# Kernel optimization log

Measured on AMD Instinct MI355X. Metric: run time of the kernel, lower is better.

Reference implementation:

```python
import jax, jax.numpy as jnp
import numpy as np

B, T, C_IN, H, NC = 256, 512, 64, 256, 6


def setup_inputs() -> dict:
    key = jax.random.key(0)
    ks = jax.random.split(key, 12)
    s = 0.05  # init scale for stability
    return {
        "x":    jax.random.normal(ks[0], (B, T, C_IN), dtype=jnp.float32),
        "Wih0": jax.random.normal(ks[1], (4 * H, C_IN), dtype=jnp.float32) * s,
        "Whh0": jax.random.normal(ks[2], (4 * H, H), dtype=jnp.float32) * s,
        "bih0": jax.random.normal(ks[3], (4 * H,), dtype=jnp.float32) * s,
        "bhh0": jax.random.normal(ks[4], (4 * H,), dtype=jnp.float32) * s,
        "Wih1": jax.random.normal(ks[5], (4 * H, H), dtype=jnp.float32) * s,
        "Whh1": jax.random.normal(ks[6], (4 * H, H), dtype=jnp.float32) * s,
        "bih1": jax.random.normal(ks[7], (4 * H,), dtype=jnp.float32) * s,
        "bhh1": jax.random.normal(ks[8], (4 * H,), dtype=jnp.float32) * s,
        "Wfc":  jax.random.normal(ks[9], (NC, H), dtype=jnp.float32) * s,
        "bfc":  jax.random.normal(ks[10], (NC,), dtype=jnp.float32) * s,
    }


def _lstm_layer(x, Wih, Whh, bih, bhh):
    # x: [B, T, D] batch_first. PyTorch/DPLSTM gate order: i, f, g, o.
    Bb, Tt, _ = x.shape
    Hh = Whh.shape[1]
    # Precompute input projections for all timesteps (one big GEMM): [T, B, 4H]
    xg = jnp.einsum('btd,gd->tbg', x, Wih) + (bih + bhh)

    def step(carry, xg_t):
        h, c = carry
        gates = xg_t + h @ Whh.T  # [B, 4H]
        i, f, g, o = jnp.split(gates, 4, axis=-1)
        i = jax.nn.sigmoid(i)
        f = jax.nn.sigmoid(f)
        g = jnp.tanh(g)
        o = jax.nn.sigmoid(o)
        c = f * c + i * g
        h = o * jnp.tanh(c)
        return (h, c), h

    h0 = jnp.zeros((Bb, Hh), dtype=x.dtype)
    c0 = jnp.zeros((Bb, Hh), dtype=x.dtype)
    _, hs = jax.lax.scan(step, (h0, c0), xg)  # hs: [T, B, H]
    return jnp.swapaxes(hs, 0, 1)  # [B, T, H]


def reference(x, Wih0, Whh0, bih0, bhh0, Wih1, Whh1, bih1, bhh1, Wfc, bfc):
    # 2-layer DPLSTM (inter-layer dropout p=0.0 -> identity, eval mode)
    h1 = _lstm_layer(x, Wih0, Whh0, bih0, bhh0)
    h2 = _lstm_layer(h1, Wih1, Whh1, bih1, bhh1)
    # Dropout(p=0.0) -> identity; Linear over all timesteps, then last step
    out = h2 @ Wfc.T + bfc           # [B, T, NC]
    logits = out[:, -1, :]           # [B, NC]
    return jax.nn.softmax(logits, axis=1)
```

## Files before the change

### kernel.cpp

```cpp
#include <hip/hip_runtime.h>
#include <stdint.h>

#define B_   256
#define T_   512
#define CIN  64
#define H_   256
#define G4   1024
#define NC   6

#define MB   32
#define NHU  16
#define NBG  (B_/MB)
#define NHG  (H_/NHU)
#define NWG  (NBG*NHG)

typedef __bf16 bf16x8 __attribute__((ext_vector_type(8)));
typedef __bf16 bf16x4 __attribute__((ext_vector_type(4)));
typedef float  f32x4  __attribute__((ext_vector_type(4)));

#define OFF_XBF   ((size_t)0)
#define SZ_XBF    ((size_t)B_*T_*CIN*2)
#define OFF_W0X   (OFF_XBF + SZ_XBF)
#define SZ_W0X    ((size_t)G4*CIN*2)
#define OFF_W0H   (OFF_W0X + SZ_W0X)
#define SZ_WH     ((size_t)G4*H_*2)
#define OFF_W1X   (OFF_W0H + SZ_WH)
#define OFF_W1H   (OFF_W1X + SZ_WH)
#define OFF_B0    (OFF_W1H + SZ_WH)
#define OFF_B1    (OFF_B0 + 4096)
#define OFF_APUB  (OFF_B1 + 4096)
#define SZ_PUB    ((size_t)2*B_*H_*2)
#define OFF_BPUB  (OFF_APUB + SZ_PUB)
#define OFF_FLAGS (OFF_BPUB + SZ_PUB)

#define DYN_LDS_ELEMS (4096 + 3*16384)
#define DYN_LDS_BYTES (DYN_LDS_ELEMS*2)

__device__ __forceinline__ f32x4 MFMA(bf16x8 a, bf16x8 b, f32x4 c) {
  return __builtin_amdgcn_mfma_f32_16x16x32_bf16(a, b, c, 0, 0, 0);
}
__device__ __forceinline__ float fsig(float x) { return 1.f/(1.f + __expf(-x)); }
__device__ __forceinline__ float ftanh_(float x) {
  float xx = fminf(fmaxf(x, -15.f), 15.f);
  float t = __expf(2.f*xx);
  return (t-1.f)/(t+1.f);
}

__device__ __forceinline__ void load8_sys(const __bf16* b, bf16x8 (&r)[8]) {
  const __bf16 *p0=b,      *p1=b+32,  *p2=b+64,  *p3=b+96,
               *p4=b+128,  *p5=b+160, *p6=b+192, *p7=b+224;
  asm volatile(
    "global_load_dwordx4 %0, %8, off sc0 sc1\n\t"
    "global_load_dwordx4 %1, %9, off sc0 sc1\n\t"
    "global_load_dwordx4 %2, %10, off sc0 sc1\n\t"
    "global_load_dwordx4 %3, %11, off sc0 sc1\n\t"
    "global_load_dwordx4 %4, %12, off sc0 sc1\n\t"
    "global_load_dwordx4 %5, %13, off sc0 sc1\n\t"
    "global_load_dwordx4 %6, %14, off sc0 sc1\n\t"
    "global_load_dwordx4 %7, %15, off sc0 sc1"
    : "=&v"(r[0]), "=&v"(r[1]), "=&v"(r[2]), "=&v"(r[3]),
      "=&v"(r[4]), "=&v"(r[5]), "=&v"(r[6]), "=&v"(r[7])
    : "v"(p0), "v"(p1), "v"(p2), "v"(p3), "v"(p4), "v"(p5), "v"(p6), "v"(p7)
    : "memory");
}
__device__ __forceinline__ void waitv0() { asm volatile("s_waitcnt vmcnt(0)" ::: "memory"); }
__device__ __forceinline__ void sbar0()  { __builtin_amdgcn_sched_barrier(0); }
__device__ __forceinline__ void store_h16(__bf16* p, float v) {
  __bf16 h = (__bf16)v;
  unsigned u = (unsigned)__builtin_bit_cast(unsigned short, h);
  asm volatile("global_store_short %0, %1, off sc0 sc1 nt" :: "v"(p), "v"(u) : "memory");
}

__global__ void k_prep_x(const float* __restrict__ x, __bf16* __restrict__ xbf) {
  int i = blockIdx.x * blockDim.x + threadIdx.x;
  const int n4 = (B_*T_*CIN)/4;
  if (i >= n4) return;
  float4 v = reinterpret_cast<const float4*>(x)[i];
  bf16x4 o;
  o[0] = (__bf16)v.x; o[1] = (__bf16)v.y; o[2] = (__bf16)v.z; o[3] = (__bf16)v.w;
  reinterpret_cast<bf16x4*>(xbf)[i] = o;
}

__global__ void k_prep_w(const float* __restrict__ Wih0, const float* __restrict__ Whh0,
                         const float* __restrict__ Wih1, const float* __restrict__ Whh1,
                         __bf16* __restrict__ w0x, __bf16* __restrict__ w0h,
                         __bf16* __restrict__ w1x, __bf16* __restrict__ w1h) {
  int e = blockIdx.x * blockDim.x + threadIdx.x;
  const int E0 = G4*CIN, E1 = G4*H_;
  const float* W; __bf16* dst; int K; int idx;
  if      (e < E0)        { W = Wih0; dst = w0x; K = CIN; idx = e; }
  else if (e < E0+E1)     { W = Whh0; dst = w0h; K = H_;  idx = e - E0; }
  else if (e < E0+2*E1)   { W = Wih1; dst = w1x; K = H_;  idx = e - E0 - E1; }
  else if (e < E0+3*E1)   { W = Whh1; dst = w1h; K = H_;  idx = e - E0 - 2*E1; }
  else return;
  const int kb = K >> 5;
  int j   = idx & 7;
  int cl  = (idx >> 3) & 15;
  int sb  = (idx >> 7) & 3;
  int ks  = (idx >> 9) % kb;
  int ct  = (idx / (512*kb)) & 3;
  int hj  =  idx / (2048*kb);
  int g  = ct*256 + hj*16 + cl;
  int kk = ks*32 + sb*8 + j;
  dst[idx] = (__bf16)W[(size_t)g*K + kk];
}

__global__ void k_prep_misc(const float* __restrict__ bih0, const float* __restrict__ bhh0,
                            const float* __restrict__ bih1, const float* __restrict__ bhh1,
                            float* __restrict__ bias0, float* __restrict__ bias1,
                            unsigned* __restrict__ zbase, unsigned* __restrict__ flags) {
  int i = blockIdx.x * blockDim.x + threadIdx.x;
  if (i < G4) bias0[i] = bih0[i] + bhh0[i];
  else if (i < 2*G4) { int j = i - G4; bias1[j] = bih1[j] + bhh1[j]; }
  int zi = i - 2*G4;
  if (zi >= 0 && zi < (int)((2*SZ_PUB)/4)) zbase[zi] = 0u;
  if (i < 128) flags[i] = 0u;
}

__global__ void __launch_bounds__(256, 1) k_lstm(
    const __bf16* __restrict__ xbf,
    const __bf16* __restrict__ w0x_g, const __bf16* __restrict__ w0h_g,
    const __bf16* __restrict__ w1x_g, const __bf16* __restrict__ w1h_g,
    const float* __restrict__ bias0, const float* __restrict__ bias1,
    __bf16* __restrict__ apub, __bf16* __restrict__ bpub,
    unsigned* __restrict__ flags,
    const float* __restrict__ Wfc, const float* __restrict__ bfc,
    float* __restrict__ out)
{
  extern __shared__ __bf16 lds[];
  __bf16* l0x = lds;
  __bf16* l0h = lds + 4096;
  __bf16* l1x = lds + 20480;
  __bf16* l1h = lds + 36864;
  __shared__ float s_log[MB][NC];

  const int tid   = threadIdx.x;
  const int bid   = blockIdx.x;
  const int bg    = bid & 7;
  const int hj    = bid >> 3;
  const int wave  = tid >> 6;
  const int lane  = tid & 63;
  const int layer = wave >> 1;
  const int mt    = wave & 1;
  const int col   = lane & 15;
  const int sub   = lane >> 4;
  const int brow  = bg*MB + mt*16;

  {
    const uint4* s; uint4* d;
    s = (const uint4*)(w0x_g + (size_t)hj*4096);  d = (uint4*)l0x;
    for (int i = tid; i < 512;  i += 256) d[i] = s[i];
    s = (const uint4*)(w0h_g + (size_t)hj*16384); d = (uint4*)l0h;
    for (int i = tid; i < 2048; i += 256) d[i] = s[i];
    s = (const uint4*)(w1x_g + (size_t)hj*16384); d = (uint4*)l1x;
    for (int i = tid; i < 2048; i += 256) d[i] = s[i];
    s = (const uint4*)(w1h_g + (size_t)hj*16384); d = (uint4*)l1h;
    for (int i = tid; i < 2048; i += 256) d[i] = s[i];
  }
  __syncthreads();

  float bs0, bs1, bs2, bs3;
  {
    const float* bp = layer ? bias1 : bias0;
    bs0 = bp[0*256 + hj*16 + col];
    bs1 = bp[1*256 + hj*16 + col];
    bs2 = bp[2*256 + hj*16 + col];
    bs3 = bp[3*256 + hj*16 + col];
  }
  float cst[4] = {0.f, 0.f, 0.f, 0.f};
  unsigned* cntp = flags + (size_t)bg*16;

  for (int k = 0; k <= T_; ++k) {
    const __bf16* a_prev = apub + (size_t)((k+1)&1)*(B_*H_);
    const __bf16* b_prev = bpub + (size_t)((k+1)&1)*(B_*H_);
    __bf16* a_cur = apub + (size_t)(k&1)*(B_*H_);
    __bf16* b_cur = bpub + (size_t)(k&1)*(B_*H_);
    const bool act0 = (layer == 0) && (k < T_);
    const bool act1 = (layer == 1) && (k >= 1);
    f32x4 acc0 = {0,0,0,0}, acc1 = {0,0,0,0}, acc2 = {0,0,0,0}, acc3 = {0,0,0,0};

    if (act0) {
      const __bf16* xr = xbf + ((size_t)(brow+col)*T_ + k)*CIN + sub*8;
      const __bf16* wb = l0x + sub*128 + col*8;
#pragma unroll
      for (int ks = 0; ks < 2; ++ks) {
        bf16x8 a = *(const bf16x8*)(xr + ks*32);
        acc0 = MFMA(a, *(const bf16x8*)(wb + ks*512 +    0), acc0);
        acc1 = MFMA(a, *(const bf16x8*)(wb + ks*512 + 1024), acc1);
        acc2 = MFMA(a, *(const bf16x8*)(wb + ks*512 + 2048), acc2);
        acc3 = MFMA(a, *(const bf16x8*)(wb + ks*512 + 3072), acc3);
      }
    }

    if (k > 0) {
      if (tid == 0) {
        const unsigned tgt = 16u * (unsigned)k;
        while (__hip_atomic_load(cntp, __ATOMIC_RELAXED, __HIP_MEMORY_SCOPE_AGENT) < tgt)
          __builtin_amdgcn_s_sleep(1);
      }
      __syncthreads();
    }

    if (act0) {
      bf16x8 ra[8];
      load8_sys(a_prev + (size_t)(brow+col)*H_ + sub*8, ra);
      waitv0(); sbar0();
      const __bf16* wb = l0h + sub*128 + col*8;
#pragma unroll
      for (int ks = 0; ks < 8; ++ks) {
        acc0 = MFMA(ra[ks], *(const bf16x8*)(wb + ks*512 +     0), acc0);
        acc1 = MFMA(ra[ks], *(const bf16x8*)(wb + ks*512 +  4096), acc1);
        acc2 = MFMA(ra[ks], *(const bf16x8*)(wb + ks*512 +  8192), acc2);
        acc3 = MFMA(ra[ks], *(const bf16x8*)(wb + ks*512 + 12288), acc3);
      }
    } else if (act1) {
      bf16x8 ra[8], rb[8];
      load8_sys(a_prev + (size_t)(brow+col)*H_ + sub*8, ra);
      load8_sys(b_prev + (size_t)(brow+col)*H_ + sub*8, rb);
      waitv0(); sbar0();
      const __bf16* w1 = l1x + sub*128 + col*8;
      const __bf16* w2 = l1h + sub*128 + col*8;
#pragma unroll
      for (int ks = 0; ks < 8; ++ks) {
        acc0 = MFMA(ra[ks], *(const bf16x8*)(w1 + ks*512 +     0), acc0);
        acc1 = MFMA(ra[ks], *(const bf16x8*)(w1 + ks*512 +  4096), acc1);
        acc2 = MFMA(ra[ks], *(const bf16x8*)(w1 + ks*512 +  8192), acc2);
        acc3 = MFMA(ra[ks], *(const bf16x8*)(w1 + ks*512 + 12288), acc3);
      }
#pragma unroll
      for (int ks = 0; ks < 8; ++ks) {
        acc0 = MFMA(rb[ks], *(const bf16x8*)(w2 + ks*512 +     0), acc0);
        acc1 = MFMA(rb[ks], *(const bf16x8*)(w2 + ks*512 +  4096), acc1);
        acc2 = MFMA(rb[ks], *(const bf16x8*)(w2 + ks*512 +  8192), acc2);
        acc3 = MFMA(rb[ks], *(const bf16x8*)(w2 + ks*512 + 12288), acc3);
      }
    }

    if (act0 || act1) {
      __bf16* dst  = act0 ? a_cur : b_cur;
      __bf16* drow = dst + (size_t)(brow + sub*4)*H_ + hj*NHU + col;
#pragma unroll
      for (int q = 0; q < 4; ++q) {
        float gi = acc0[q] + bs0;
        float gf = acc1[q] + bs1;
        float gg = acc2[q] + bs2;
        float go = acc3[q] + bs3;
        float si = fsig(gi), sf = fsig(gf), sg = ftanh_(gg), so = fsig(go);
        float c = sf*cst[q] + si*sg;
        cst[q] = c;
        store_h16(drow + (size_t)q*H_, so * ftanh_(c));
      }
    }

    waitv0();
    __syncthreads();
    if (tid == 0)
      __hip_atomic_fetch_add(cntp, 1u, __ATOMIC_RELAXED, __HIP_MEMORY_SCOPE_AGENT);
  }

  if (hj == 0) {
    if (tid == 0) {
      const unsigned tgt = 16u * (unsigned)(T_ + 1);
      while (__hip_atomic_load(cntp, __ATOMIC_RELAXED, __HIP_MEMORY_SCOPE_AGENT) < tgt)
        __builtin_amdgcn_s_sleep(1);
    }
    __syncthreads();
    __builtin_amdgcn_fence(__ATOMIC_ACQUIRE, "agent");
    if (tid < MB*NC) {
      int r = tid / NC, cl = tid % NC;
      const __bf16* hr = bpub + (size_t)(bg*MB + r)*H_;
      const float*  wr = Wfc + (size_t)cl*H_;
      float s = bfc[cl];
      for (int j2 = 0; j2 < H_; ++j2) s = fmaf((float)hr[j2], wr[j2], s);
      s_log[r][cl] = s;
    }
    __syncthreads();
    if (tid < MB) {
      float mx = s_log[tid][0];
#pragma unroll
      for (int c2 = 1; c2 < NC; ++c2) mx = fmaxf(mx, s_log[tid][c2]);
      float e[NC]; float se = 0.f;
#pragma unroll
      for (int c2 = 0; c2 < NC; ++c2) { e[c2] = __expf(s_log[tid][c2] - mx); se += e[c2]; }
      float inv = 1.f/se;
#pragma unroll
      for (int c2 = 0; c2 < NC; ++c2) out[(size_t)(bg*MB + tid)*NC + c2] = e[c2]*inv;
    }
  }
}

extern "C" void kernel_launch(void* const* d_in, const int* in_sizes, int n_in,
                              void* d_out, int out_size, void* d_ws, size_t ws_size,
                              hipStream_t stream) {
  const float* x    = (const float*)d_in[0];
  const float* Wih0 = (const float*)d_in[1];
  const float* Whh0 = (const float*)d_in[2];
  const float* bih0 = (const float*)d_in[3];
  const float* bhh0 = (const float*)d_in[4];
  const float* Wih1 = (const float*)d_in[5];
  const float* Whh1 = (const float*)d_in[6];
  const float* bih1 = (const float*)d_in[7];
  const float* bhh1 = (const float*)d_in[8];
  const float* Wfc  = (const float*)d_in[9];
  const float* bfc  = (const float*)d_in[10];
  float* out = (float*)d_out;
  char*  ws  = (char*)d_ws;

  __bf16* xbf  = (__bf16*)(ws + OFF_XBF);
  __bf16* w0x  = (__bf16*)(ws + OFF_W0X);
  __bf16* w0h  = (__bf16*)(ws + OFF_W0H);
  __bf16* w1x  = (__bf16*)(ws + OFF_W1X);
  __bf16* w1h  = (__bf16*)(ws + OFF_W1H);
  float*  b0   = (float*) (ws + OFF_B0);
  float*  b1   = (float*) (ws + OFF_B1);
  __bf16* apub = (__bf16*)(ws + OFF_APUB);
  __bf16* bpub = (__bf16*)(ws + OFF_BPUB);
  unsigned* flags = (unsigned*)(ws + OFF_FLAGS);

  {
    const int n4 = (B_*T_*CIN)/4;
    k_prep_x<<<(n4 + 255)/256, 256, 0, stream>>>(x, xbf);
  }
  {
    const int tot = G4*CIN + 3*G4*H_;
    k_prep_w<<<(tot + 255)/256, 256, 0, stream>>>(Wih0, Whh0, Wih1, Whh1, w0x, w0h, w1x, w1h);
  }
  {
    const int tot = 2*G4 + (int)((2*SZ_PUB)/4);
    k_prep_misc<<<(tot + 255)/256, 256, 0, stream>>>(bih0, bhh0, bih1, bhh1, b0, b1,
                                                     (unsigned*)apub, flags);
  }
  (void)hipFuncSetAttribute((const void*)k_lstm,
                            hipFuncAttributeMaxDynamicSharedMemorySize, DYN_LDS_BYTES);
  k_lstm<<<NWG, 256, DYN_LDS_BYTES, stream>>>(xbf, w0x, w0h, w1x, w1h, b0, b1,
                                              apub, bpub, flags, Wfc, bfc, out);
}
```

Measured before the change: 2.460 ms.

## Replace block barriers with per-wave, per-layer counters and 4-slot hidden-state ring

```diff
diff --git a/kernel.cpp b/kernel.cpp
--- a/kernel.cpp
+++ b/kernel.cpp
@@ -13,6 +13,7 @@
 #define NBG  (B_/MB)
 #define NHG  (H_/NHU)
 #define NWG  (NBG*NHG)
+#define SLOTS 4
 
 typedef __bf16 bf16x8 __attribute__((ext_vector_type(8)));
 typedef __bf16 bf16x4 __attribute__((ext_vector_type(4)));
@@ -29,9 +30,10 @@
 #define OFF_B0    (OFF_W1H + SZ_WH)
 #define OFF_B1    (OFF_B0 + 4096)
 #define OFF_APUB  (OFF_B1 + 4096)
-#define SZ_PUB    ((size_t)2*B_*H_*2)
+#define SZ_PUB    ((size_t)SLOTS*B_*H_*2)
 #define OFF_BPUB  (OFF_APUB + SZ_PUB)
-#define OFF_FLAGS (OFF_BPUB + SZ_PUB)
+#define OFF_SYNC  (OFF_BPUB + SZ_PUB)
+#define SYNC_WORDS 4096
 
 #define DYN_LDS_ELEMS (4096 + 3*16384)
 #define DYN_LDS_BYTES (DYN_LDS_ELEMS*2)
@@ -46,7 +48,7 @@
   return (t-1.f)/(t+1.f);
 }
 
-__device__ __forceinline__ void load8_sys(const __bf16* b, bf16x8 (&r)[8]) {
+__device__ __forceinline__ void load8_c(const __bf16* b, bf16x8 (&r)[8]) {
   const __bf16 *p0=b,      *p1=b+32,  *p2=b+64,  *p3=b+96,
                *p4=b+128,  *p5=b+160, *p6=b+192, *p7=b+224;
   asm volatile(
@@ -65,10 +67,17 @@
 }
 __device__ __forceinline__ void waitv0() { asm volatile("s_waitcnt vmcnt(0)" ::: "memory"); }
 __device__ __forceinline__ void sbar0()  { __builtin_amdgcn_sched_barrier(0); }
-__device__ __forceinline__ void store_h16(__bf16* p, float v) {
-  __bf16 h = (__bf16)v;
-  unsigned u = (unsigned)__builtin_bit_cast(unsigned short, h);
-  asm volatile("global_store_short %0, %1, off sc0 sc1 nt" :: "v"(p), "v"(u) : "memory");
+
+__device__ __forceinline__ void pollAB(const unsigned* p, unsigned tA, unsigned tB) {
+  const unsigned long long* q = (const unsigned long long*)p;
+  for (;;) {
+    unsigned long long v = __hip_atomic_load(q, __ATOMIC_RELAXED, __HIP_MEMORY_SCOPE_AGENT);
+    if ((unsigned)v >= tA && (unsigned)(v >> 32) >= tB) return;
+    __builtin_amdgcn_s_sleep(1);
+  }
+}
+__device__ __forceinline__ void st8_pub(__bf16* p, uint2 v) {
+  asm volatile("global_store_dwordx2 %0, %1, off sc0 sc1" :: "v"(p), "v"(v) : "memory");
 }
 
 __global__ void k_prep_x(const float* __restrict__ x, __bf16* __restrict__ xbf) {
@@ -108,13 +117,15 @@
 __global__ void k_prep_misc(const float* __restrict__ bih0, const float* __restrict__ bhh0,
                             const float* __restrict__ bih1, const float* __restrict__ bhh1,
                             float* __restrict__ bias0, float* __restrict__ bias1,
-                            unsigned* __restrict__ zbase, unsigned* __restrict__ flags) {
+                            unsigned* __restrict__ zpub, unsigned* __restrict__ syncw) {
   int i = blockIdx.x * blockDim.x + threadIdx.x;
   if (i < G4) bias0[i] = bih0[i] + bhh0[i];
   else if (i < 2*G4) { int j = i - G4; bias1[j] = bih1[j] + bhh1[j]; }
+  const int PW = (int)((2*SZ_PUB)/4);
   int zi = i - 2*G4;
-  if (zi >= 0 && zi < (int)((2*SZ_PUB)/4)) zbase[zi] = 0u;
-  if (i < 128) flags[i] = 0u;
+  if (zi >= 0 && zi < PW) zpub[zi] = 0u;
+  int zf = i - 2*G4 - PW;
+  if (zf >= 0 && zf < SYNC_WORDS) syncw[zf] = 0u;
 }
 
 __global__ void __launch_bounds__(256, 1) k_lstm(
@@ -123,7 +134,7 @@
     const __bf16* __restrict__ w1x_g, const __bf16* __restrict__ w1h_g,
     const float* __restrict__ bias0, const float* __restrict__ bias1,
     __bf16* __restrict__ apub, __bf16* __restrict__ bpub,
-    unsigned* __restrict__ flags,
+    unsigned* __restrict__ sync,
     const float* __restrict__ Wfc, const float* __restrict__ bfc,
     float* __restrict__ out)
 {
@@ -132,7 +143,8 @@
   __bf16* l0h = lds + 4096;
   __bf16* l1x = lds + 20480;
   __bf16* l1h = lds + 36864;
-  __shared__ float s_log[MB][NC];
+  __shared__ float  s_log[MB][NC];
+  __shared__ __bf16 s_stage[4][16][16];
 
   const int tid   = threadIdx.x;
   const int bid   = blockIdx.x;
@@ -146,6 +158,8 @@
   const int sub   = lane >> 4;
   const int brow  = bg*MB + mt*16;
 
+  unsigned* cnt = sync + (size_t)bg*32;
+
   {
     const uint4* s; uint4* d;
     s = (const uint4*)(w0x_g + (size_t)hj*4096);  d = (uint4*)l0x;
@@ -168,13 +182,8 @@
     bs3 = bp[3*256 + hj*16 + col];
   }
   float cst[4] = {0.f, 0.f, 0.f, 0.f};
-  unsigned* cntp = flags + (size_t)bg*16;
 
   for (int k = 0; k <= T_; ++k) {
-    const __bf16* a_prev = apub + (size_t)((k+1)&1)*(B_*H_);
-    const __bf16* b_prev = bpub + (size_t)((k+1)&1)*(B_*H_);
-    __bf16* a_cur = apub + (size_t)(k&1)*(B_*H_);
-    __bf16* b_cur = bpub + (size_t)(k&1)*(B_*H_);
     const bool act0 = (layer == 0) && (k < T_);
     const bool act1 = (layer == 1) && (k >= 1);
     f32x4 acc0 = {0,0,0,0}, acc1 = {0,0,0,0}, acc2 = {0,0,0,0}, acc3 = {0,0,0,0};
@@ -192,18 +201,21 @@
       }
     }
 
-    if (k > 0) {
-      if (tid == 0) {
-        const unsigned tgt = 16u * (unsigned)k;
-        while (__hip_atomic_load(cntp, __ATOMIC_RELAXED, __HIP_MEMORY_SCOPE_AGENT) < tgt)
-          __builtin_amdgcn_s_sleep(1);
-      }
-      __syncthreads();
-    }
-
     if (act0) {
+      if (k > 0) {
+        unsigned tA = 32u * (unsigned)k;
+        unsigned tB = (k >= 2) ? 32u * (unsigned)(k-2) : 0u;
+        pollAB(cnt, tA, tB);
+      }
+    } else if (act1) {
+      unsigned t = 32u * (unsigned)k;
+      pollAB(cnt, t, t);
+    }
+
+    if (act0) {
+      const __bf16* a_prev = apub + (size_t)((k-1)&3)*(B_*H_);
       bf16x8 ra[8];
-      load8_sys(a_prev + (size_t)(brow+col)*H_ + sub*8, ra);
+      load8_c(a_prev + (size_t)(brow+col)*H_ + sub*8, ra);
       waitv0(); sbar0();
       const __bf16* wb = l0h + sub*128 + col*8;
 #pragma unroll
@@ -214,9 +226,11 @@
         acc3 = MFMA(ra[ks], *(const bf16x8*)(wb + ks*512 + 12288), acc3);
       }
     } else if (act1) {
+      const __bf16* a_prev = apub + (size_t)((k-1)&3)*(B_*H_);
+      const __bf16* b_prev = bpub + (size_t)((k-2)&3)*(B_*H_);
       bf16x8 ra[8], rb[8];
-      load8_sys(a_prev + (size_t)(brow+col)*H_ + sub*8, ra);
-      load8_sys(b_prev + (size_t)(brow+col)*H_ + sub*8, rb);
+      load8_c(a_prev + (size_t)(brow+col)*H_ + sub*8, ra);
+      load8_c(b_prev + (size_t)(brow+col)*H_ + sub*8, rb);
       waitv0(); sbar0();
       const __bf16* w1 = l1x + sub*128 + col*8;
       const __bf16* w2 = l1h + sub*128 + col*8;
@@ -237,8 +251,8 @@
     }
 
     if (act0 || act1) {
-      __bf16* dst  = act0 ? a_cur : b_cur;
-      __bf16* drow = dst + (size_t)(brow + sub*4)*H_ + hj*NHU + col;
+      const int slot = act0 ? (k & 3) : ((k - 1) & 3);
+      __bf16* dst = (act0 ? apub : bpub) + (size_t)slot*(B_*H_);
 #pragma unroll
       for (int q = 0; q < 4; ++q) {
         float gi = acc0[q] + bs0;
@@ -248,30 +262,36 @@
         float si = fsig(gi), sf = fsig(gf), sg = ftanh_(gg), so = fsig(go);
         float c = sf*cst[q] + si*sg;
         cst[q] = c;
-        store_h16(drow + (size_t)q*H_, so * ftanh_(c));
-      }
+        s_stage[wave][sub*4+q][col] = (__bf16)(so * ftanh_(c));
+      }
+      asm volatile("s_waitcnt lgkmcnt(0)" ::: "memory");
+      sbar0();
+      const int r16 = lane >> 2, seg = lane & 3;
+      uint2 packed = *reinterpret_cast<const uint2*>(&s_stage[wave][r16][seg*4]);
+      __bf16* pa = dst + (size_t)(bg*MB + mt*16 + r16)*H_ + hj*16 + seg*4;
+      st8_pub(pa, packed);
     }
 
     waitv0();
-    __syncthreads();
-    if (tid == 0)
-      __hip_atomic_fetch_add(cntp, 1u, __ATOMIC_RELAXED, __HIP_MEMORY_SCOPE_AGENT);
+    if (lane == 0)
+      __hip_atomic_fetch_add(cnt + layer, 1u, __ATOMIC_RELAXED, __HIP_MEMORY_SCOPE_AGENT);
   }
 
   if (hj == 0) {
-    if (tid == 0) {
-      const unsigned tgt = 16u * (unsigned)(T_ + 1);
-      while (__hip_atomic_load(cntp, __ATOMIC_RELAXED, __HIP_MEMORY_SCOPE_AGENT) < tgt)
-        __builtin_amdgcn_s_sleep(1);
-    }
-    __syncthreads();
-    __builtin_amdgcn_fence(__ATOMIC_ACQUIRE, "agent");
+    pollAB(cnt, 0u, 32u * (unsigned)(T_ + 1));
     if (tid < MB*NC) {
       int r = tid / NC, cl = tid % NC;
-      const __bf16* hr = bpub + (size_t)(bg*MB + r)*H_;
+      const __bf16* hr = bpub + (size_t)((T_-1)&3)*(B_*H_) + (size_t)(bg*MB + r)*H_;
       const float*  wr = Wfc + (size_t)cl*H_;
       float s = bfc[cl];
-      for (int j2 = 0; j2 < H_; ++j2) s = fmaf((float)hr[j2], wr[j2], s);
+      for (int c8 = 0; c8 < 32; ++c8) {
+        bf16x8 v;
+        const __bf16* p = hr + c8*8;
+        asm volatile("global_load_dwordx4 %0, %1, off sc0 sc1\n\ts_waitcnt vmcnt(0)"
+                     : "=&v"(v) : "v"(p) : "memory");
+#pragma unroll
+        for (int j = 0; j < 8; ++j) s = fmaf((float)v[j], wr[c8*8+j], s);
+      }
       s_log[r][cl] = s;
     }
     __syncthreads();
@@ -315,7 +335,7 @@
   float*  b1   = (float*) (ws + OFF_B1);
   __bf16* apub = (__bf16*)(ws + OFF_APUB);
   __bf16* bpub = (__bf16*)(ws + OFF_BPUB);
-  unsigned* flags = (unsigned*)(ws + OFF_FLAGS);
+  unsigned* syncw = (unsigned*)(ws + OFF_SYNC);
 
   {
     const int n4 = (B_*T_*CIN)/4;
@@ -326,12 +346,12 @@
     k_prep_w<<<(tot + 255)/256, 256, 0, stream>>>(Wih0, Whh0, Wih1, Whh1, w0x, w0h, w1x, w1h);
   }
   {
-    const int tot = 2*G4 + (int)((2*SZ_PUB)/4);
+    const int tot = 2*G4 + (int)((2*SZ_PUB)/4) + SYNC_WORDS;
     k_prep_misc<<<(tot + 255)/256, 256, 0, stream>>>(bih0, bhh0, bih1, bhh1, b0, b1,
-                                                     (unsigned*)apub, flags);
+                                                     (unsigned*)apub, syncw);
   }
   (void)hipFuncSetAttribute((const void*)k_lstm,
                             hipFuncAttributeMaxDynamicSharedMemorySize, DYN_LDS_BYTES);
   k_lstm<<<NWG, 256, DYN_LDS_BYTES, stream>>>(xbf, w0x, w0h, w1x, w1h, b0, b1,
-                                              apub, bpub, flags, Wfc, bfc, out);
-}
+                                              apub, bpub, syncw, Wfc, bfc, out);
+}
```

After: 3.401 ms. 38.3% more time.

## Replace atomic counter barrier with per-workgroup stamp flags polled in parallel

Applied to the files above, without the earlier changes.

```diff
diff --git a/kernel.cpp b/kernel.cpp
--- a/kernel.cpp
+++ b/kernel.cpp
@@ -31,7 +31,8 @@
 #define OFF_APUB  (OFF_B1 + 4096)
 #define SZ_PUB    ((size_t)2*B_*H_*2)
 #define OFF_BPUB  (OFF_APUB + SZ_PUB)
-#define OFF_FLAGS (OFF_BPUB + SZ_PUB)
+#define OFF_SYNC  (OFF_BPUB + SZ_PUB)
+#define SYNC_WORDS 512
 
 #define DYN_LDS_ELEMS (4096 + 3*16384)
 #define DYN_LDS_BYTES (DYN_LDS_ELEMS*2)
@@ -46,7 +47,7 @@
   return (t-1.f)/(t+1.f);
 }
 
-__device__ __forceinline__ void load8_sys(const __bf16* b, bf16x8 (&r)[8]) {
+__device__ __forceinline__ void load8_c(const __bf16* b, bf16x8 (&r)[8]) {
   const __bf16 *p0=b,      *p1=b+32,  *p2=b+64,  *p3=b+96,
                *p4=b+128,  *p5=b+160, *p6=b+192, *p7=b+224;
   asm volatile(
@@ -65,10 +66,24 @@
 }
 __device__ __forceinline__ void waitv0() { asm volatile("s_waitcnt vmcnt(0)" ::: "memory"); }
 __device__ __forceinline__ void sbar0()  { __builtin_amdgcn_sched_barrier(0); }
+
+__device__ __forceinline__ void poll16(const unsigned* fb, unsigned tgt) {
+  const unsigned* p = fb + (threadIdx.x & 15);
+  for (;;) {
+    unsigned v;
+    asm volatile("global_load_dword %0, %1, off sc0 sc1\n\ts_waitcnt vmcnt(0)"
+                 : "=&v"(v) : "v"(p) : "memory");
+    if (__ballot(v >= tgt) == ~0ull) return;
+    __builtin_amdgcn_s_sleep(1);
+  }
+}
+__device__ __forceinline__ void store_stamp(unsigned* p, unsigned v) {
+  asm volatile("global_store_dword %0, %1, off sc0 sc1" :: "v"(p), "v"(v) : "memory");
+}
 __device__ __forceinline__ void store_h16(__bf16* p, float v) {
   __bf16 h = (__bf16)v;
   unsigned u = (unsigned)__builtin_bit_cast(unsigned short, h);
-  asm volatile("global_store_short %0, %1, off sc0 sc1 nt" :: "v"(p), "v"(u) : "memory");
+  asm volatile("global_store_short %0, %1, off sc0 sc1" :: "v"(p), "v"(u) : "memory");
 }
 
 __global__ void k_prep_x(const float* __restrict__ x, __bf16* __restrict__ xbf) {
@@ -108,13 +123,14 @@
 __global__ void k_prep_misc(const float* __restrict__ bih0, const float* __restrict__ bhh0,
                             const float* __restrict__ bih1, const float* __restrict__ bhh1,
                             float* __restrict__ bias0, float* __restrict__ bias1,
-                            unsigned* __restrict__ zbase, unsigned* __restrict__ flags) {
+                            unsigned* __restrict__ zpub, unsigned* __restrict__ syncw) {
   int i = blockIdx.x * blockDim.x + threadIdx.x;
   if (i < G4) bias0[i] = bih0[i] + bhh0[i];
   else if (i < 2*G4) { int j = i - G4; bias1[j] = bih1[j] + bhh1[j]; }
+  const int PW = (int)((2*SZ_PUB)/4);
   int zi = i - 2*G4;
-  if (zi >= 0 && zi < (int)((2*SZ_PUB)/4)) zbase[zi] = 0u;
-  if (i < 128) flags[i] = 0u;
+  if (zi >= 0 && zi < PW) zpub[zi] = 0u;
+  if (i < SYNC_WORDS) syncw[i] = 0u;
 }
 
 __global__ void __launch_bounds__(256, 1) k_lstm(
@@ -123,7 +139,7 @@
     const __bf16* __restrict__ w1x_g, const __bf16* __restrict__ w1h_g,
     const float* __restrict__ bias0, const float* __restrict__ bias1,
     __bf16* __restrict__ apub, __bf16* __restrict__ bpub,
-    unsigned* __restrict__ flags,
+    unsigned* __restrict__ sync,
     const float* __restrict__ Wfc, const float* __restrict__ bfc,
     float* __restrict__ out)
 {
@@ -146,6 +162,9 @@
   const int sub   = lane >> 4;
   const int brow  = bg*MB + mt*16;
 
+  unsigned* stline = sync + (size_t)bg*64;
+  unsigned* myst   = stline + hj;
+
   {
     const uint4* s; uint4* d;
     s = (const uint4*)(w0x_g + (size_t)hj*4096);  d = (uint4*)l0x;
@@ -168,7 +187,6 @@
     bs3 = bp[3*256 + hj*16 + col];
   }
   float cst[4] = {0.f, 0.f, 0.f, 0.f};
-  unsigned* cntp = flags + (size_t)bg*16;
 
   for (int k = 0; k <= T_; ++k) {
     const __bf16* a_prev = apub + (size_t)((k+1)&1)*(B_*H_);
@@ -193,17 +211,13 @@
     }
 
     if (k > 0) {
-      if (tid == 0) {
-        const unsigned tgt = 16u * (unsigned)k;
-        while (__hip_atomic_load(cntp, __ATOMIC_RELAXED, __HIP_MEMORY_SCOPE_AGENT) < tgt)
-          __builtin_amdgcn_s_sleep(1);
-      }
+      if (tid < 64) poll16(stline, (unsigned)k);
       __syncthreads();
     }
 
     if (act0) {
       bf16x8 ra[8];
-      load8_sys(a_prev + (size_t)(brow+col)*H_ + sub*8, ra);
+      load8_c(a_prev + (size_t)(brow+col)*H_ + sub*8, ra);
       waitv0(); sbar0();
       const __bf16* wb = l0h + sub*128 + col*8;
 #pragma unroll
@@ -215,8 +229,8 @@
       }
     } else if (act1) {
       bf16x8 ra[8], rb[8];
-      load8_sys(a_prev + (size_t)(brow+col)*H_ + sub*8, ra);
-      load8_sys(b_prev + (size_t)(brow+col)*H_ + sub*8, rb);
+      load8_c(a_prev + (size_t)(brow+col)*H_ + sub*8, ra);
+      load8_c(b_prev + (size_t)(brow+col)*H_ + sub*8, rb);
       waitv0(); sbar0();
       const __bf16* w1 = l1x + sub*128 + col*8;
       const __bf16* w2 = l1h + sub*128 + col*8;
@@ -254,24 +268,25 @@
 
     waitv0();
     __syncthreads();
-    if (tid == 0)
-      __hip_atomic_fetch_add(cntp, 1u, __ATOMIC_RELAXED, __HIP_MEMORY_SCOPE_AGENT);
+    if (tid == 0) store_stamp(myst, (unsigned)(k + 1));
   }
 
   if (hj == 0) {
-    if (tid == 0) {
-      const unsigned tgt = 16u * (unsigned)(T_ + 1);
-      while (__hip_atomic_load(cntp, __ATOMIC_RELAXED, __HIP_MEMORY_SCOPE_AGENT) < tgt)
-        __builtin_amdgcn_s_sleep(1);
-    }
+    if (tid < 64) poll16(stline, (unsigned)(T_ + 1));
     __syncthreads();
-    __builtin_amdgcn_fence(__ATOMIC_ACQUIRE, "agent");
     if (tid < MB*NC) {
       int r = tid / NC, cl = tid % NC;
       const __bf16* hr = bpub + (size_t)(bg*MB + r)*H_;
       const float*  wr = Wfc + (size_t)cl*H_;
       float s = bfc[cl];
-      for (int j2 = 0; j2 < H_; ++j2) s = fmaf((float)hr[j2], wr[j2], s);
+      for (int c8 = 0; c8 < 32; ++c8) {
+        bf16x8 v;
+        const __bf16* p = hr + c8*8;
+        asm volatile("global_load_dwordx4 %0, %1, off sc0 sc1\n\ts_waitcnt vmcnt(0)"
+                     : "=&v"(v) : "v"(p) : "memory");
+#pragma unroll
+        for (int j = 0; j < 8; ++j) s = fmaf((float)v[j], wr[c8*8+j], s);
+      }
       s_log[r][cl] = s;
     }
     __syncthreads();
@@ -315,7 +330,7 @@
   float*  b1   = (float*) (ws + OFF_B1);
   __bf16* apub = (__bf16*)(ws + OFF_APUB);
   __bf16* bpub = (__bf16*)(ws + OFF_BPUB);
-  unsigned* flags = (unsigned*)(ws + OFF_FLAGS);
+  unsigned* syncw = (unsigned*)(ws + OFF_SYNC);
 
   {
     const int n4 = (B_*T_*CIN)/4;
@@ -328,10 +343,10 @@
   {
     const int tot = 2*G4 + (int)((2*SZ_PUB)/4);
     k_prep_misc<<<(tot + 255)/256, 256, 0, stream>>>(bih0, bhh0, bih1, bhh1, b0, b1,
-                                                     (unsigned*)apub, flags);
+                                                     (unsigned*)apub, syncw);
   }
   (void)hipFuncSetAttribute((const void*)k_lstm,
                             hipFuncAttributeMaxDynamicSharedMemorySize, DYN_LDS_BYTES);
   k_lstm<<<NWG, 256, DYN_LDS_BYTES, stream>>>(xbf, w0x, w0h, w1x, w1h, b0, b1,
-                                              apub, bpub, flags, Wfc, bfc, out);
-}
+                                              apub, bpub, syncw, Wfc, bfc, out);
+}
```

New measurement: 2.609 ms. 6.1% more time.
